# Optimization experiments

Hardware: AMD Instinct MI355X
Metric: run time of the kernel (lower is better)

Reference implementation:

```python
import jax, jax.numpy as jnp
import numpy as np

B, H, W = 4, 192, 192
CIN, CB, CM = 64, 16, 256   # backbone out, bottleneck, mask channels
TOPK = 16
TEMP = 1.0
COLOR_NORM = 1.0
BN_EPS = 1e-5


def setup_inputs() -> dict:
    key = jax.random.key(0)
    k0, k1, k2, k3 = jax.random.split(key, 4)
    img = jax.random.uniform(k0, (B, 3, H, W), jnp.float32)
    base_feat = jax.random.normal(k1, (B, CIN, H, W), jnp.float32)
    w_bneck = jax.random.normal(k2, (CB, CIN), jnp.float32) * 0.05
    b_bneck = jnp.zeros((CB,), jnp.float32)
    bn_gamma = jnp.ones((CB,), jnp.float32)
    bn_beta = jnp.zeros((CB,), jnp.float32)
    w_mask = jax.random.normal(k3, (CM, CB), jnp.float32) * 0.05
    return dict(img=img, base_feat=base_feat, w_bneck=w_bneck, b_bneck=b_bneck,
                bn_gamma=bn_gamma, bn_beta=bn_beta, w_mask=w_mask, num_colors=256)


def reference(img, base_feat, w_bneck, b_bneck, bn_gamma, bn_beta, w_mask, num_colors):
    b, _, h, w = img.shape
    # bottleneck: 1x1 conv + BatchNorm (training batch stats) + ReLU
    x = jnp.einsum('bchw,oc->bohw', base_feat, w_bneck) + b_bneck[None, :, None, None]
    mean = x.mean(axis=(0, 2, 3))
    var = x.var(axis=(0, 2, 3))
    x = (x - mean[None, :, None, None]) * jax.lax.rsqrt(var + BN_EPS)[None, :, None, None]
    feat = jax.nn.relu(x * bn_gamma[None, :, None, None] + bn_beta[None, :, None, None])
    # color mask: 1x1 conv (no bias) -> [B, 256, H, W]
    m = jnp.einsum('bchw,oc->bohw', feat, w_mask)
    # fold 256 channels into num_colors groups and sum -> [B, K, H, W]
    m = m.reshape(b, -1, num_colors, h, w).sum(axis=1)
    k = min(TOPK, num_colors)
    # top-k over the color axis, softmax, scatter back into sparse mask
    mt = jnp.transpose(m, (0, 2, 3, 1))              # [B, H, W, K]
    vals, idx = jax.lax.top_k(mt, k)                 # [B, H, W, k]
    sm = jax.nn.softmax(vals / TEMP, axis=-1)
    m_sp = jnp.zeros_like(mt).at[
        jnp.arange(b)[:, None, None, None],
        jnp.arange(h)[None, :, None, None],
        jnp.arange(w)[None, None, :, None],
        idx].set(sm)
    m_sp = jnp.transpose(m_sp, (0, 3, 1, 2))         # [B, K, H, W]
    # weighted color palette: avoid the [B,3,K,H,W] intermediate via einsum
    num = jnp.einsum('bchw,bkhw->bck', img, m_sp)    # [B, 3, K]
    den = m_sp.sum(axis=(2, 3))[:, None, :] + 1e-8   # [B, 1, K]
    color_palette = num / den / COLOR_NORM           # [B, 3, K]
    transformed_img = jnp.einsum('bkhw,bck->bchw', m_sp, color_palette)
    return transformed_img, m_sp, color_palette[:, :, :, None, None]
```

## Files before the change

### kernel.cpp

```cpp
#include <hip/hip_runtime.h>

#define HW    36864
#define NB    4
#define NCH   256
#define CIN   64
#define CB    16
#define NPIX  (NB*HW)
#define DELTA 1e-4f

typedef short bf16x8 __attribute__((ext_vector_type(8)));
typedef float f32x4  __attribute__((ext_vector_type(4)));

struct FlagEntry {
  unsigned pix;
  unsigned char cnt, need, r0, r1;
  unsigned char ks[8];
};


__device__ __forceinline__ unsigned short bf16_rne(float x) {
  unsigned u = __float_as_uint(x);
  unsigned r = u + 0x7fffu + ((u >> 16) & 1u);
  return (unsigned short)(r >> 16);
}
__device__ __forceinline__ float bf16_tof(unsigned short h) {
  return __uint_as_float(((unsigned)h) << 16);
}


template<bool ASC>
__device__ __forceinline__ void bitonic16(float* v) {
  #pragma unroll
  for (int K = 2; K <= 16; K <<= 1) {
    #pragma unroll
    for (int J = K >> 1; J > 0; J >>= 1) {
      #pragma unroll
      for (int i = 0; i < 16; ++i) {
        int l = i ^ J;
        if (l > i) {
          bool up = (((i & K) == 0) == ASC);
          float a = v[i], b = v[l];
          float lo = fminf(a, b), hi = fmaxf(a, b);
          v[i] = up ? lo : hi;
          v[l] = up ? hi : lo;
        }
      }
    }
  }
}

__device__ __forceinline__ void bmerge16_desc(float* v) {
  #pragma unroll
  for (int J = 8; J > 0; J >>= 1) {
    #pragma unroll
    for (int i = 0; i < 16; ++i) {
      int l = i ^ J;
      if (l > i) {
        float a = v[i], b = v[l];
        float lo = fminf(a, b), hi = fmaxf(a, b);
        v[i] = hi; v[l] = lo;
      }
    }
  }
}


__global__ void k0_zero(unsigned* flagcnt) { *flagcnt = 0u; }


__global__ __launch_bounds__(256) void k1_conv(
    const float* __restrict__ bfeat, const float* __restrict__ wb,
    const float* __restrict__ bb, float* __restrict__ xout,
    double* __restrict__ part)
{
  __shared__ float wbT[CIN][CB];
  __shared__ double redS[4][CB];
  __shared__ double redQ[4][CB];
  const int t = threadIdx.x;
  for (int i = t; i < CIN*CB; i += 256) {
    int o = i >> 6, c = i & 63;
    wbT[c][o] = wb[i];
  }
  __syncthreads();

  const int blk = blockIdx.x;
  const int b = blk / 144, seg = blk % 144;
  const int p = seg * 256 + t;
  const float* bfb = bfeat + (size_t)b * CIN * HW;

  float acc[CB];
  #pragma unroll
  for (int o = 0; o < CB; ++o) acc[o] = bb[o];

  for (int c = 0; c < CIN; ++c) {
    float v = bfb[(size_t)c*HW + p];
    #pragma unroll
    for (int o4 = 0; o4 < 4; ++o4) {
      float4 w4 = *(const float4*)&wbT[c][o4*4];
      acc[o4*4+0] = fmaf(v, w4.x, acc[o4*4+0]);
      acc[o4*4+1] = fmaf(v, w4.y, acc[o4*4+1]);
      acc[o4*4+2] = fmaf(v, w4.z, acc[o4*4+2]);
      acc[o4*4+3] = fmaf(v, w4.w, acc[o4*4+3]);
    }
  }

  float* xb = xout + (size_t)b * CB * HW;
  #pragma unroll
  for (int o = 0; o < CB; ++o) xb[(size_t)o*HW + p] = acc[o];

  const int wv = t >> 6, lane = t & 63;
  #pragma unroll
  for (int o = 0; o < CB; ++o) {
    double a = (double)acc[o], q = a*a;
    for (int off = 32; off; off >>= 1) { a += __shfl_xor(a, off); q += __shfl_xor(q, off); }
    if (lane == 0) { redS[wv][o] = a; redQ[wv][o] = q; }
  }
  __syncthreads();
  if (t < CB) {
    double a = redS[0][t] + redS[1][t] + redS[2][t] + redS[3][t];
    part[(size_t)blk*32 + t] = a;
  } else if (t < 32) {
    int o = t - CB;
    double q = redQ[0][o] + redQ[1][o] + redQ[2][o] + redQ[3][o];
    part[(size_t)blk*32 + t] = q;
  }
}


__global__ __launch_bounds__(64) void k1b_stats(
    const double* __restrict__ part, const float* __restrict__ gam,
    const float* __restrict__ bet, double* __restrict__ st64, float* __restrict__ st32)
{
  __shared__ double sh[32];
  const int t = threadIdx.x;
  if (t < 32) {
    double a = 0.0;
    #pragma unroll 8
    for (int i = 0; i < 576; ++i) a += part[(size_t)i*32 + t];
    sh[t] = a;
  }
  __syncthreads();
  if (t < CB) {
    const double N = (double)NPIX;
    double mean = sh[t] / N;
    double var  = sh[16+t] / N - mean*mean;
    double rstd = 1.0 / sqrt(var + 1e-5);
    double scl = (double)gam[t] * rstd;
    double sft = (double)bet[t] - mean*scl;
    st64[t] = scl; st64[CB+t] = sft;
    st32[t] = (float)scl; st32[CB+t] = (float)sft;
  }
}


__global__ __launch_bounds__(256) void k1c_bfrag(
    const float* __restrict__ wm, short* __restrict__ bfrag)
{
  const int t = threadIdx.x;
  for (int e = t; e < 2048; e += 256) {
    const int v = e >> 10, ct = (e >> 6) & 15, l = e & 63;
    const int n = l & 15, g = l >> 4;
    const int col = ct*16 + n;
    short out[8];
    #pragma unroll
    for (int j = 0; j < 8; ++j) {
      const int k = g*8 + j;
      const int kk = k & 15;
      const bool hi_half = (k < 16);
      float w = wm[col*CB + kk];
      unsigned short hb = bf16_rne(w);
      float res = w - bf16_tof(hb);
      unsigned short lb = bf16_rne(res);
      bool use_hi = ((v == 0) == hi_half);
      out[j] = (short)(use_hi ? hb : lb);
    }
    bf16x8 pk;
    #pragma unroll
    for (int j = 0; j < 8; ++j) pk[j] = out[j];
    *(bf16x8*)&bfrag[(size_t)e * 8] = pk;
  }
}


__device__ __forceinline__ void k2_epilogue(int b, int p, int pxl,
    int selN, int nearN, int nselN,
    float* lcw, unsigned char* lidx, unsigned char* lnear,
    unsigned* cidx, float* cw, unsigned* flagcnt, FlagEntry* entries)
{
  int start = selN < 16 ? selN : 16;
  for (int j = start; j < 16; ++j) { lcw[pxl*16 + j] = 0.f; lidx[pxl*16 + j] = 0; }
  unsigned g = (unsigned)(b*HW + p);
  uint4 iv = *(uint4*)&lidx[pxl*16];
  ((uint4*)cidx)[g] = iv;
  float4* cwq = (float4*)cw;
  #pragma unroll
  for (int q = 0; q < 4; ++q) cwq[(size_t)g*4 + q] = *(float4*)&lcw[pxl*16 + q*4];
  bool flag = (nearN > 1) || (selN != 16);
  if (flag) {
    unsigned slot = atomicAdd(flagcnt, 1u);
    FlagEntry e;
    e.pix = g;
    int cnt = nearN < 8 ? nearN : 8;
    e.cnt = (unsigned char)cnt;
    int nsure = selN - nselN;
    int need = 16 - nsure;
    if (need < 0) need = 0;
    if (need > cnt) need = cnt;
    e.need = (unsigned char)need;
    e.r0 = (nearN > 8 || selN != 16) ? 1 : 0;
    e.r1 = 0;
    #pragma unroll
    for (int j = 0; j < 8; ++j) e.ks[j] = (j < cnt) ? lnear[pxl*8 + j] : 0;
    entries[slot] = e;
  }
}

#define PXW 16
#define PXB 64

__global__ __launch_bounds__(256, 3) void k2_main(
    const float* __restrict__ x, const short* __restrict__ bfrag,
    const float* __restrict__ st32, float* __restrict__ msp,
    unsigned* __restrict__ cidx, float* __restrict__ cw,
    unsigned* __restrict__ flagcnt, FlagEntry* __restrict__ entries)
{
  __shared__ short A_st[PXB*40];
  __shared__ float lcw[PXB*16];
  __shared__ __align__(16) unsigned char lidx[PXB*16];
  __shared__ unsigned char lnear[PXB*8];

  const int t = threadIdx.x;
  const int blk = blockIdx.x;
  const int b = blk / 576;
  const int p0 = (blk % 576) * PXB;
  const float* xb = x + (size_t)b*CB*HW + p0;

  #pragma unroll
  for (int r = 0; r < 4; ++r) {
    int e = r*256 + t;
    int o = e >> 6, pl = e & 63;
    float vx = xb[(size_t)o*HW + pl];
    float f = fmaxf(0.f, fmaf(vx, st32[o], st32[CB+o]));
    unsigned short hb = bf16_rne(f);
    float res = f - bf16_tof(hb);
    unsigned short lb = bf16_rne(res);
    A_st[pl*40 + o]      = (short)hb;
    A_st[pl*40 + 16 + o] = (short)lb;
  }
  __syncthreads();

  const int w = t >> 6, l = t & 63;
  const int pl15 = l & 15;
  const int q = l >> 4;
  const int px = w*PXW + pl15;
  const int p = p0 + px;

  bf16x8 a = *(const bf16x8*)&A_st[px*40 + q*8];
  float mv[64];
  #pragma unroll
  for (int ct = 0; ct < 16; ++ct) {
    bf16x8 b1 = *(const bf16x8*)&bfrag[(size_t)(ct*64 + l)*8];
    bf16x8 b2 = *(const bf16x8*)&bfrag[(size_t)((16 + ct)*64 + l)*8];
    f32x4 acc = {0.f, 0.f, 0.f, 0.f};
    acc = __builtin_amdgcn_mfma_f32_16x16x32_bf16(b1, a, acc, 0, 0, 0);
    acc = __builtin_amdgcn_mfma_f32_16x16x32_bf16(b2, a, acc, 0, 0, 0);
    mv[ct*4+0] = acc[0]; mv[ct*4+1] = acc[1];
    mv[ct*4+2] = acc[2]; mv[ct*4+3] = acc[3];
  }

  float T[16], tmp[16];
  #pragma unroll
  for (int i = 0; i < 16; ++i) tmp[i] = mv[i];
  bitonic16<false>(tmp);
  #pragma unroll
  for (int i = 0; i < 16; ++i) T[i] = tmp[i];
  #pragma unroll
  for (int c = 1; c < 4; ++c) {
    #pragma unroll
    for (int i = 0; i < 16; ++i) tmp[i] = mv[c*16 + i];
    bitonic16<true>(tmp);
    #pragma unroll
    for (int i = 0; i < 16; ++i) T[i] = fmaxf(T[i], tmp[i]);
    bmerge16_desc(T);
  }
  #pragma unroll
  for (int mk = 16; mk <= 32; mk <<= 1) {
    float R[16];
    #pragma unroll
    for (int i = 0; i < 16; ++i) R[i] = fmaxf(T[i], __shfl_xor(T[15-i], mk));
    bmerge16_desc(R);
    #pragma unroll
    for (int i = 0; i < 16; ++i) T[i] = R[i];
  }
  const float tau = T[15], top = T[0];
  float Z = 0.f;
  #pragma unroll
  for (int i = 0; i < 16; ++i) Z += __expf(T[i] - top);
  const float iZ = 1.f / Z;

  int cs = 0, cn = 0, cns = 0;
  #pragma unroll
  for (int j = 0; j < 64; ++j) {
    float v = mv[j];
    bool s = (v >= tau);
    bool nr = (fabsf(v - tau) <= DELTA);
    cs += s ? 1 : 0; cn += nr ? 1 : 0; cns += (s && nr) ? 1 : 0;
  }
  int offs = 0, offn = 0, selN = 0, nearN = 0, nselN = 0;
  #pragma unroll
  for (int q2 = 0; q2 < 4; ++q2) {
    int cv = __shfl(cs,  pl15 + 16*q2);
    int nv = __shfl(cn,  pl15 + 16*q2);
    int sv = __shfl(cns, pl15 + 16*q2);
    selN += cv; nearN += nv; nselN += sv;
    if (q2 < q) { offs += cv; offn += nv; }
  }

  float* mspb = msp + (size_t)b*NCH*HW;
  int isel = 0, inear = 0;
  #pragma unroll
  for (int ct = 0; ct < 16; ++ct) {
    #pragma unroll
    for (int i = 0; i < 4; ++i) {
      const int k = ct*16 + q*4 + i;
      const float v = mv[ct*4+i];
      const bool s = (v >= tau);
      const bool nr = (fabsf(v - tau) <= DELTA);
      float wv = s ? __expf(v - top) * iZ : 0.f;
      mspb[(size_t)k*HW + p] = wv;
      if (s) {
        int slot = offs + isel;
        if (slot < 16) { lcw[px*16 + slot] = wv; lidx[px*16 + slot] = (unsigned char)k; }
        ++isel;
      }
      if (nr) {
        int gs = offn + inear;
        if (gs < 8) lnear[px*8 + gs] = (unsigned char)k;
        ++inear;
      }
    }
  }

  if (q == 0)
    k2_epilogue(b, p, px, selN, nearN, nselN, lcw, lidx, lnear,
                cidx, cw, flagcnt, entries);
}


__global__ __launch_bounds__(64) void k2b_fix(
    const float* __restrict__ bfeat, const float* __restrict__ wb,
    const float* __restrict__ bb, const float* __restrict__ wmg,
    const double* __restrict__ st64,
    const unsigned* __restrict__ flagcnt, const FlagEntry* __restrict__ entries,
    float* __restrict__ msp, unsigned* __restrict__ cidx, float* __restrict__ cw)
{
  __shared__ float wbT[CB][CIN];
  __shared__ float  wOrigL[16];
  __shared__ int    kOrigL[16];
  __shared__ float  wnL[8];
  __shared__ int    kL[8];
  __shared__ double tvL[16];
  __shared__ int    tiL[16];
  __shared__ float  wvL[16];

  const int lane = threadIdx.x;
  for (int i = lane; i < CB*CIN; i += 64) wbT[i >> 6][i & 63] = wb[i];
  __syncthreads();

  const unsigned n = *flagcnt;
  for (unsigned idx = blockIdx.x; idx < n; idx += gridDim.x) {
    FlagEntry e = entries[idx];
    const int b = (int)(e.pix / HW), p = (int)(e.pix % HW);

    const double v = (double)bfeat[(size_t)b*CIN*HW + (size_t)lane*HW + p];
    double ft[CB];
    #pragma unroll
    for (int o = 0; o < CB; ++o) {
      double s = v * (double)wbT[o][lane];
      #pragma unroll
      for (int off = 32; off; off >>= 1) s += __shfl_xor(s, off);
      s += (double)bb[o];
      ft[o] = fmax(0.0, s*st64[o] + st64[CB+o]);
    }

    float* mb = msp + (size_t)b*NCH*HW;
    unsigned char* cb_ = (unsigned char*)cidx + (size_t)e.pix*16;
    float* cwp = cw + (size_t)e.pix*16;

    if (e.r0) {
      double mm[4]; int kk4[4];
      #pragma unroll
      for (int u = 0; u < 4; ++u) {
        const int k = lane + 64*u; kk4[u] = k;
        const float* wr = wmg + k*CB;
        double a = 0.0;
        #pragma unroll
        for (int c = 0; c < CB; ++c) a = fma(ft[c], (double)wr[c], a);
        mm[u] = a;
      }
      for (int j = 0; j < 16; ++j) {
        double bm = mm[0]; int bk = kk4[0];
        #pragma unroll
        for (int u = 1; u < 4; ++u) {
          bool gt = (mm[u] > bm) || (mm[u] == bm && kk4[u] < bk);
          if (gt) { bm = mm[u]; bk = kk4[u]; }
        }
        #pragma unroll
        for (int off = 32; off; off >>= 1) {
          double om = __shfl_xor(bm, off);
          int ok = __shfl_xor(bk, off);
          bool gt = (om > bm) || (om == bm && ok < bk);
          if (gt) { bm = om; bk = ok; }
        }
        if (lane == 0) { tvL[j] = bm; tiL[j] = bk; }
        #pragma unroll
        for (int u = 0; u < 4; ++u) if (kk4[u] == bk) mm[u] = -1.0e300;
      }
      __syncthreads();
      const double top = tvL[0];
      double ej = (lane < 16) ? exp(tvL[lane] - top) : 0.0;
      double Z = ej;
      #pragma unroll
      for (int off = 32; off; off >>= 1) Z += __shfl_xor(Z, off);
      if (lane < 16) wvL[lane] = (float)(ej / Z);
      __syncthreads();
      int tiR[16]; float wvR[16];
      #pragma unroll
      for (int j = 0; j < 16; ++j) { tiR[j] = tiL[j]; wvR[j] = wvL[j]; }
      #pragma unroll
      for (int u = 0; u < 4; ++u) {
        const int k = lane + 64*u;
        float wv = 0.f;
        #pragma unroll
        for (int j = 0; j < 16; ++j) if (tiR[j] == k) wv = wvR[j];
        mb[(size_t)k*HW + p] = wv;
      }
      if (lane == 0) {
        unsigned used = 0; int on = 0;
        for (int it = 0; it < 16; ++it) {
          int bk = 1 << 20;
          #pragma unroll
          for (int j = 0; j < 16; ++j)
            if (!((used >> j) & 1u) && tiR[j] < bk) bk = tiR[j];
          if (bk >= (1 << 20)) break;
          float bw = 0.f;
          #pragma unroll
          for (int j = 0; j < 16; ++j)
            if (tiR[j] == bk) { bw = wvR[j]; used |= (1u << j); }
          if (bw != 0.f && on < 16) { cb_[on] = (unsigned char)bk; cwp[on] = bw; ++on; }
        }
        for (int j = on; j < 16; ++j) { cb_[j] = 0; cwp[j] = 0.f; }
      }
      __syncthreads();
      continue;
    }

    const int cnt = (e.cnt > 8) ? 8 : (int)e.cnt;
    int need = (int)e.need; if (need > cnt) need = cnt;

    if (lane < 16) { wOrigL[lane] = cwp[lane]; kOrigL[lane] = (int)cb_[lane]; }
    __syncthreads();

    const int myk = (lane < cnt) ? (int)e.ks[lane] : 0x7fffffff;
    double mj = 0.0;
    if (lane < cnt) {
      const float* wr = wmg + myk*CB;
      #pragma unroll
      for (int c = 0; c < CB; ++c) mj = fma(ft[c], (double)wr[c], mj);
    }
    float woldj = 0.f;
    if (lane < cnt) {
      #pragma unroll
      for (int q = 0; q < 16; ++q) {
        if (kOrigL[q] == myk && wOrigL[q] > 0.f) woldj = wOrigL[q];
      }
    }
    int rankj = 0;
    #pragma unroll
    for (int j2 = 0; j2 < 8; ++j2) {
      double m2 = __shfl(mj, j2);
      int k2v = __shfl(myk, j2);
      if (lane < cnt && j2 < cnt && j2 != lane) {
        bool gt = (m2 > mj) || (m2 == mj && k2v < myk);
        rankj += gt ? 1 : 0;
      }
    }
    float w2[8];
    #pragma unroll
    for (int j2 = 0; j2 < 8; ++j2) w2[j2] = __shfl(woldj, j2);
    int nw = 0;
    #pragma unroll
    for (int j2 = 0; j2 < 8; ++j2) if (j2 < cnt && w2[j2] > 0.f) ++nw;
    float wnj = 0.f;
    if (lane < cnt && rankj < need && rankj < nw) {
      #pragma unroll
      for (int cand = 0; cand < 8; ++cand) {
        if (cand < cnt && w2[cand] > 0.f) {
          float xv = w2[cand];
          int cgt = 0, cge = 0;
          #pragma unroll
          for (int j2 = 0; j2 < 8; ++j2)
            if (j2 < cnt && w2[j2] > 0.f) { cgt += (w2[j2] > xv); cge += (w2[j2] >= xv); }
          if (cgt <= rankj && rankj < cge) wnj = xv;
        }
      }
    }
    if (lane < cnt) mb[(size_t)myk*HW + p] = wnj;
    if (lane < 8)  { wnL[lane] = wnj; kL[lane] = myk; }
    __syncthreads();

    if (lane == 0) {
      unsigned char nk[16]; float nwv[16];
      int on = 0;
      for (int j = 0; j < 16; ++j) {
        int ko = kOrigL[j]; float wo = wOrigL[j];
        if (wo <= 0.f) continue;
        bool isNear = false;
        #pragma unroll
        for (int j2 = 0; j2 < 8; ++j2)
          if (j2 < cnt && kL[j2] == ko) isNear = true;
        if (isNear) continue;
        if (on < 16) { nk[on] = (unsigned char)ko; nwv[on] = wo; ++on; }
      }
      for (int j2 = 0; j2 < 8; ++j2)
        if (j2 < cnt && wnL[j2] > 0.f && on < 16) {
          nk[on] = (unsigned char)kL[j2]; nwv[on] = wnL[j2]; ++on;
        }
      for (int j = 0; j < on; ++j) { cb_[j] = nk[j]; cwp[j] = nwv[j]; }
      for (int j = on; j < 16; ++j) { cb_[j] = 0; cwp[j] = 0.f; }
    }
    __syncthreads();
  }
}


__global__ __launch_bounds__(256) void k3_accum(
    const uint4* __restrict__ cidx, const float4* __restrict__ cw4,
    const float* __restrict__ img, float* __restrict__ part)
{
  __shared__ float acc[1024];
  const int t = threadIdx.x, blk = blockIdx.x;
  for (int i = t; i < 1024; i += 256) acc[i] = 0.f;
  __syncthreads();
  const int b = blk / 144;
  const int p = (blk % 144) * 256 + t;
  const float* imb = img + (size_t)b*3*HW;
  const int g = b*HW + p;
  uint4 iv = cidx[g];
  unsigned ivq[4] = {iv.x, iv.y, iv.z, iv.w};
  float r = imb[p], g_ = imb[HW + p], bl = imb[2*HW + p];
  #pragma unroll
  for (int q = 0; q < 4; ++q) {
    float4 wv = cw4[(size_t)g*4 + q];
    float wvv[4] = {wv.x, wv.y, wv.z, wv.w};
    #pragma unroll
    for (int u = 0; u < 4; ++u) {
      int k = (int)((ivq[q] >> (8*u)) & 255u);
      float wgt = wvv[u];
      atomicAdd(&acc[k],       wgt * r);
      atomicAdd(&acc[256 + k], wgt * g_);
      atomicAdd(&acc[512 + k], wgt * bl);
      atomicAdd(&acc[768 + k], wgt);
    }
  }
  __syncthreads();
  for (int i = t; i < 1024; i += 256) part[(size_t)blk*1024 + i] = acc[i];
}


__global__ __launch_bounds__(256) void k4_pal(
    const float* __restrict__ part, float* __restrict__ out_pal)
{
  __shared__ float acc[1024];
  const int b = blockIdx.x, t = threadIdx.x;
  for (int s = t; s < 1024; s += 256) {
    float a = 0.f;
    for (int i = 0; i < 144; ++i) a += part[(size_t)(b*144 + i)*1024 + s];
    acc[s] = a;
  }
  __syncthreads();
  for (int s = t; s < 768; s += 256) {
    int k = s & 255;
    float den = acc[768 + k] + 1e-8f;
    out_pal[(size_t)b*768 + s] = acc[s] / den;
  }
}


__global__ __launch_bounds__(256) void k5_img(
    const uint4* __restrict__ cidx, const float4* __restrict__ cw4,
    const float* __restrict__ pal, float* __restrict__ outimg)
{
  __shared__ float lp[768];
  const int t = threadIdx.x, blk = blockIdx.x;
  const int b = blk / 144;
  for (int i = t; i < 768; i += 256) lp[i] = pal[(size_t)b*768 + i];
  __syncthreads();
  const int p = (blk % 144) * 256 + t;
  const int g = b*HW + p;
  uint4 iv = cidx[g];
  unsigned ivq[4] = {iv.x, iv.y, iv.z, iv.w};
  float r = 0.f, g_ = 0.f, bl = 0.f;
  #pragma unroll
  for (int q = 0; q < 4; ++q) {
    float4 wv = cw4[(size_t)g*4 + q];
    float wvv[4] = {wv.x, wv.y, wv.z, wv.w};
    #pragma unroll
    for (int u = 0; u < 4; ++u) {
      int k = (int)((ivq[q] >> (8*u)) & 255u);
      float wgt = wvv[u];
      r  = fmaf(wgt, lp[k],       r);
      g_ = fmaf(wgt, lp[256 + k], g_);
      bl = fmaf(wgt, lp[512 + k], bl);
    }
  }
  float* ob = outimg + (size_t)b*3*HW;
  ob[p] = r; ob[HW + p] = g_; ob[2*HW + p] = bl;
}


extern "C" void kernel_launch(void* const* d_in, const int* in_sizes, int n_in,
                              void* d_out, int out_size, void* d_ws, size_t ws_size,
                              hipStream_t stream)
{
  const float* img   = (const float*)d_in[0];
  const float* bfeat = (const float*)d_in[1];
  const float* wb    = (const float*)d_in[2];
  const float* bb    = (const float*)d_in[3];
  const float* gam   = (const float*)d_in[4];
  const float* bet   = (const float*)d_in[5];
  const float* wm    = (const float*)d_in[6];

  float* out_img = (float*)d_out;
  float* out_msp = (float*)d_out + 442368;
  float* out_pal = (float*)d_out + 38191104;

  char* w = (char*)d_ws;
  float*     ws_x       = (float*)(w);
  double*    ws_part    = (double*)(w + 9437184);
  double*    ws_st64    = (double*)(w + 9584640);
  float*     ws_st32    = (float*)(w + 9584896);
  unsigned*  ws_flagcnt = (unsigned*)(w + 9585152);
  FlagEntry* ws_entries = (FlagEntry*)(w + 9585408);
  unsigned*  ws_cidx    = (unsigned*)(w + 11944704);
  float*     ws_cw      = (float*)(w + 14304000);
  float*     ws_nd      = ws_x;
  short*     ws_bfrag   = (short*)(w + 23741184);

  k0_zero<<<dim3(1), dim3(1), 0, stream>>>(ws_flagcnt);
  k1_conv<<<dim3(576), dim3(256), 0, stream>>>(bfeat, wb, bb, ws_x, ws_part);
  k1b_stats<<<dim3(1), dim3(64), 0, stream>>>(ws_part, gam, bet, ws_st64, ws_st32);
  k1c_bfrag<<<dim3(1), dim3(256), 0, stream>>>(wm, ws_bfrag);
  k2_main<<<dim3(2304), dim3(256), 0, stream>>>(ws_x, ws_bfrag, ws_st32, out_msp,
                                                ws_cidx, ws_cw, ws_flagcnt, ws_entries);
  k2b_fix<<<dim3(4096), dim3(64), 0, stream>>>(bfeat, wb, bb, wm, ws_st64,
                                               ws_flagcnt, ws_entries, out_msp, ws_cidx, ws_cw);
  k3_accum<<<dim3(576), dim3(256), 0, stream>>>((const uint4*)ws_cidx, (const float4*)ws_cw,
                                                img, ws_nd);
  k4_pal<<<dim3(4), dim3(256), 0, stream>>>(ws_nd, out_pal);
  k5_img<<<dim3(576), dim3(256), 0, stream>>>((const uint4*)ws_cidx, (const float4*)ws_cw,
                                              out_pal, out_img);
}
```

Baseline: 297.5 us.

## Merge small setup kernels and privatize palette accumulators per wavefront

Folds the flag-zeroing, BN-stats and weight-fragment kernels into one two-block auxiliary kernel, cutting two launches and running the stats and fragment work in parallel blocks. The stats reduction now splits across 256 threads with a shared-memory reduction instead of 32 threads each looping serially. The palette accumulation kernel gives each wavefront its own LDS histogram copy to reduce atomic contention, summed at the end. The palette reduction kernel keeps its sums in registers instead of staging them in shared memory. The cost is four times the LDS use in the accumulation kernel.

```diff
diff --git a/kernel.cpp b/kernel.cpp
--- a/kernel.cpp
+++ b/kernel.cpp
@@ -65,9 +65,6 @@
 }
 
 
-__global__ void k0_zero(unsigned* flagcnt) { *flagcnt = 0u; }
-
-
 __global__ __launch_bounds__(256) void k1_conv(
     const float* __restrict__ bfeat, const float* __restrict__ wb,
     const float* __restrict__ bb, float* __restrict__ xout,
@@ -127,57 +124,62 @@
 }
 
 
-__global__ __launch_bounds__(64) void k1b_stats(
+__global__ __launch_bounds__(256) void k1x_aux(
     const double* __restrict__ part, const float* __restrict__ gam,
-    const float* __restrict__ bet, double* __restrict__ st64, float* __restrict__ st32)
-{
-  __shared__ double sh[32];
+    const float* __restrict__ bet, double* __restrict__ st64,
+    float* __restrict__ st32, const float* __restrict__ wm,
+    short* __restrict__ bfrag, unsigned* __restrict__ flagcnt)
+{
   const int t = threadIdx.x;
-  if (t < 32) {
+  if (blockIdx.x == 0) {
+    if (t == 0) *flagcnt = 0u;
+    __shared__ double red[8][32];
+    const int g = t >> 5, ch = t & 31;
     double a = 0.0;
     #pragma unroll 8
-    for (int i = 0; i < 576; ++i) a += part[(size_t)i*32 + t];
-    sh[t] = a;
-  }
-  __syncthreads();
-  if (t < CB) {
-    const double N = (double)NPIX;
-    double mean = sh[t] / N;
-    double var  = sh[16+t] / N - mean*mean;
-    double rstd = 1.0 / sqrt(var + 1e-5);
-    double scl = (double)gam[t] * rstd;
-    double sft = (double)bet[t] - mean*scl;
-    st64[t] = scl; st64[CB+t] = sft;
-    st32[t] = (float)scl; st32[CB+t] = (float)sft;
-  }
-}
-
-
-__global__ __launch_bounds__(256) void k1c_bfrag(
-    const float* __restrict__ wm, short* __restrict__ bfrag)
-{
-  const int t = threadIdx.x;
-  for (int e = t; e < 2048; e += 256) {
-    const int v = e >> 10, ct = (e >> 6) & 15, l = e & 63;
-    const int n = l & 15, g = l >> 4;
-    const int col = ct*16 + n;
-    short out[8];
-    #pragma unroll
-    for (int j = 0; j < 8; ++j) {
-      const int k = g*8 + j;
-      const int kk = k & 15;
-      const bool hi_half = (k < 16);
-      float w = wm[col*CB + kk];
-      unsigned short hb = bf16_rne(w);
-      float res = w - bf16_tof(hb);
-      unsigned short lb = bf16_rne(res);
-      bool use_hi = ((v == 0) == hi_half);
-      out[j] = (short)(use_hi ? hb : lb);
-    }
-    bf16x8 pk;
-    #pragma unroll
-    for (int j = 0; j < 8; ++j) pk[j] = out[j];
-    *(bf16x8*)&bfrag[(size_t)e * 8] = pk;
+    for (int i = g; i < 576; i += 8) a += part[(size_t)i*32 + ch];
+    red[g][ch] = a;
+    __syncthreads();
+    if (t < 32) {
+      double s = 0.0;
+      #pragma unroll
+      for (int g2 = 0; g2 < 8; ++g2) s += red[g2][t];
+      red[0][t] = s;
+    }
+    __syncthreads();
+    if (t < CB) {
+      const double N = (double)NPIX;
+      double mean = red[0][t] / N;
+      double var  = red[0][16+t] / N - mean*mean;
+      double rstd = 1.0 / sqrt(var + 1e-5);
+      double scl = (double)gam[t] * rstd;
+      double sft = (double)bet[t] - mean*scl;
+      st64[t] = scl; st64[CB+t] = sft;
+      st32[t] = (float)scl; st32[CB+t] = (float)sft;
+    }
+  } else {
+    for (int e = t; e < 2048; e += 256) {
+      const int v = e >> 10, ct = (e >> 6) & 15, l = e & 63;
+      const int n = l & 15, g = l >> 4;
+      const int col = ct*16 + n;
+      short out[8];
+      #pragma unroll
+      for (int j = 0; j < 8; ++j) {
+        const int k = g*8 + j;
+        const int kk = k & 15;
+        const bool hi_half = (k < 16);
+        float w = wm[col*CB + kk];
+        unsigned short hb = bf16_rne(w);
+        float res = w - bf16_tof(hb);
+        unsigned short lb = bf16_rne(res);
+        bool use_hi = ((v == 0) == hi_half);
+        out[j] = (short)(use_hi ? hb : lb);
+      }
+      bf16x8 pk;
+      #pragma unroll
+      for (int j = 0; j < 8; ++j) pk[j] = out[j];
+      *(bf16x8*)&bfrag[(size_t)e * 8] = pk;
+    }
   }
 }
 
@@ -538,10 +540,11 @@
     const uint4* __restrict__ cidx, const float4* __restrict__ cw4,
     const float* __restrict__ img, float* __restrict__ part)
 {
-  __shared__ float acc[1024];
+  __shared__ float acc[4][1024];
   const int t = threadIdx.x, blk = blockIdx.x;
-  for (int i = t; i < 1024; i += 256) acc[i] = 0.f;
+  for (int i = t; i < 4096; i += 256) ((float*)acc)[i] = 0.f;
   __syncthreads();
+  const int wv = t >> 6;
   const int b = blk / 144;
   const int p = (blk % 144) * 256 + t;
   const float* imb = img + (size_t)b*3*HW;
@@ -551,39 +554,37 @@
   float r = imb[p], g_ = imb[HW + p], bl = imb[2*HW + p];
   #pragma unroll
   for (int q = 0; q < 4; ++q) {
-    float4 wv = cw4[(size_t)g*4 + q];
-    float wvv[4] = {wv.x, wv.y, wv.z, wv.w};
+    float4 wvv4 = cw4[(size_t)g*4 + q];
+    float wvv[4] = {wvv4.x, wvv4.y, wvv4.z, wvv4.w};
     #pragma unroll
     for (int u = 0; u < 4; ++u) {
       int k = (int)((ivq[q] >> (8*u)) & 255u);
       float wgt = wvv[u];
-      atomicAdd(&acc[k],       wgt * r);
-      atomicAdd(&acc[256 + k], wgt * g_);
-      atomicAdd(&acc[512 + k], wgt * bl);
-      atomicAdd(&acc[768 + k], wgt);
+      atomicAdd(&acc[wv][k],       wgt * r);
+      atomicAdd(&acc[wv][256 + k], wgt * g_);
+      atomicAdd(&acc[wv][512 + k], wgt * bl);
+      atomicAdd(&acc[wv][768 + k], wgt);
     }
   }
   __syncthreads();
-  for (int i = t; i < 1024; i += 256) part[(size_t)blk*1024 + i] = acc[i];
+  for (int i = t; i < 1024; i += 256)
+    part[(size_t)blk*1024 + i] = (acc[0][i] + acc[1][i]) + (acc[2][i] + acc[3][i]);
 }
 
 
 __global__ __launch_bounds__(256) void k4_pal(
     const float* __restrict__ part, float* __restrict__ out_pal)
 {
-  __shared__ float acc[1024];
   const int b = blockIdx.x, t = threadIdx.x;
-  for (int s = t; s < 1024; s += 256) {
-    float a = 0.f;
-    for (int i = 0; i < 144; ++i) a += part[(size_t)(b*144 + i)*1024 + s];
-    acc[s] = a;
-  }
-  __syncthreads();
-  for (int s = t; s < 768; s += 256) {
-    int k = s & 255;
-    float den = acc[768 + k] + 1e-8f;
-    out_pal[(size_t)b*768 + s] = acc[s] / den;
-  }
+  float ar = 0.f, ag = 0.f, ab = 0.f, aw = 0.f;
+  for (int i = 0; i < 144; ++i) {
+    const float* pp = part + (size_t)(b*144 + i)*1024;
+    ar += pp[t]; ag += pp[256 + t]; ab += pp[512 + t]; aw += pp[768 + t];
+  }
+  float den = aw + 1e-8f;
+  out_pal[(size_t)b*768 + t]       = ar / den;
+  out_pal[(size_t)b*768 + 256 + t] = ag / den;
+  out_pal[(size_t)b*768 + 512 + t] = ab / den;
 }
 
 
@@ -647,10 +648,9 @@
   float*     ws_nd      = ws_x;
   short*     ws_bfrag   = (short*)(w + 23741184);
 
-  k0_zero<<<dim3(1), dim3(1), 0, stream>>>(ws_flagcnt);
   k1_conv<<<dim3(576), dim3(256), 0, stream>>>(bfeat, wb, bb, ws_x, ws_part);
-  k1b_stats<<<dim3(1), dim3(64), 0, stream>>>(ws_part, gam, bet, ws_st64, ws_st32);
-  k1c_bfrag<<<dim3(1), dim3(256), 0, stream>>>(wm, ws_bfrag);
+  k1x_aux<<<dim3(2), dim3(256), 0, stream>>>(ws_part, gam, bet, ws_st64, ws_st32,
+                                             wm, ws_bfrag, ws_flagcnt);
   k2_main<<<dim3(2304), dim3(256), 0, stream>>>(ws_x, ws_bfrag, ws_st32, out_msp,
                                                 ws_cidx, ws_cw, ws_flagcnt, ws_entries);
   k2b_fix<<<dim3(4096), dim3(64), 0, stream>>>(bfeat, wb, bb, wm, ws_st64,
```

Result: faster. 262.4 us (median of 3 runs) (-11.8%).
